# Optimization experiments

Measured on AMD Instinct MI355X. Metric: run time of the kernel, lower is better.

## Reference

```python
import jax, jax.numpy as jnp
import numpy as np

B, L, H, E = 2, 2048, 16, 64  # S == L (causal self-attention), D == E


def setup_inputs() -> dict:
    key = jax.random.key(0)
    kq, kk, kv, ks = jax.random.split(key, 4)
    queries = jax.random.normal(kq, (B, L, H, E), dtype=jnp.float32)
    keys = jax.random.normal(kk, (B, L, H, E), dtype=jnp.float32)
    values = jax.random.normal(kv, (B, L, H, E), dtype=jnp.float32)
    # TriangularCausalMask: True above the diagonal -> masked out
    attn_mask = jnp.broadcast_to(
        jnp.triu(jnp.ones((L, L), dtype=bool), k=1)[None, None], (B, 1, L, L)
    )
    init_score = jax.random.uniform(ks, (B, L, L), dtype=jnp.float32)
    return {
        "queries": queries,
        "keys": keys,
        "values": values,
        "attn_mask": attn_mask,
        "init_score": init_score,
    }


def reference(queries, keys, values, attn_mask, init_score):
    # queries: [B,L,H,E], keys: [B,S,H,E], values: [B,S,H,D]
    E_ = queries.shape[-1]
    scale = 1.0 / np.sqrt(E_).astype(np.float32)
    # scores: [B,H,L,S]
    scores = jnp.einsum('blhe,bshe->bhls', queries, keys)
    scores = jnp.where(attn_mask, -jnp.inf, scores)
    A = jax.nn.softmax(scale * scores, axis=-1)  # dropout p=0 -> identity
    # post-softmax bias, broadcast over heads
    A = A + 0.1 * init_score[:, None, :, :]
    # V: [B,L,H,D]
    V = jnp.einsum('bhls,bshd->blhd', A, values)
    return V
```

## Files before the change

### kernel.cpp

```cpp
#include <hip/hip_runtime.h>
#include <hip/hip_bf16.h>
#include <math.h>

#define BB 2
#define LL 2048
#define HH 16
#define EE 64
#define LOG2E 1.44269504089f

typedef __attribute__((ext_vector_type(8))) short short8;
typedef __attribute__((ext_vector_type(4))) float floatx4;
typedef unsigned int u32;

union S8 { short8 v; u32 u[4]; ushort4 q[2]; };

__device__ inline u32 pkbf(float lo, float hi) {
    union { __hip_bfloat162 h; u32 u; } c;
    c.h = __float22bfloat162_rn(make_float2(lo, hi));
    return c.u;
}

__device__ inline ushort4 cvt4(float4 v) {
    union { __hip_bfloat162 h; u32 u; } a, b;
    a.h = __float22bfloat162_rn(make_float2(v.x, v.y));
    b.h = __float22bfloat162_rn(make_float2(v.z, v.w));
    ushort4 r;
    r.x = (unsigned short)(a.u & 0xffffu);
    r.y = (unsigned short)(a.u >> 16);
    r.z = (unsigned short)(b.u & 0xffffu);
    r.w = (unsigned short)(b.u >> 16);
    return r;
}

__device__ inline short8 pack8(float4 a, float4 b) {
    S8 s; s.q[0] = cvt4(a); s.q[1] = cvt4(b); return s.v;
}

__device__ inline void async16(unsigned short* lds, const unsigned short* g) {
    __builtin_amdgcn_global_load_lds(
        (const __attribute__((address_space(1))) u32*)g,
        (__attribute__((address_space(3))) u32*)lds, 16, 0, 0);
}

__global__ __launch_bounds__(256) void prepass(
    const float* __restrict__ k, const float* __restrict__ v,
    const float* __restrict__ isc, unsigned short* __restrict__ kb,
    unsigned short* __restrict__ vt, unsigned short* __restrict__ isb)
{
    const int bid = blockIdx.x;
    const int t = threadIdx.x;
    if (bid < 1024) {
        #pragma unroll
        for (int it = 0; it < 2; ++it) {
            int idx = bid * 512 + it * 256 + t;
            const float4* src = (const float4*)k + idx * 2;
            float4 a = src[0], c = src[1];
            int e8 = idx & 7, h = (idx >> 3) & 15, l = (idx >> 7) & 2047, b = idx >> 18;
            *(short8*)&kb[(((b * 16 + h) * 2048 + l) * 64) + e8 * 8] = pack8(a, c);
        }
    } else if (bid < 2048) {
        __shared__ float Tf[64][69];
        const int vb = bid - 1024;
        const int st = vb & 31, h = (vb >> 5) & 15, b = vb >> 9;
        const int s0 = st * 64;
        #pragma unroll
        for (int i = 0; i < 4; ++i) {
            int r = i * 16 + (t >> 4), c = (t & 15) * 4;
            float4 val = *(const float4*)(v + (((b * LL + s0 + r) * HH + h) * EE) + c);
            *(float4*)&Tf[r][c] = val;
        }
        __syncthreads();
        #pragma unroll
        for (int i = 0; i < 2; ++i) {
            int slot = t + i * 256;
            int d = slot >> 3, s8 = (slot & 7) * 8;
            float4 lo = make_float4(Tf[s8 + 0][d], Tf[s8 + 1][d],
                                    Tf[s8 + 2][d], Tf[s8 + 3][d]);
            float4 hi = make_float4(Tf[s8 + 4][d], Tf[s8 + 5][d],
                                    Tf[s8 + 6][d], Tf[s8 + 7][d]);
            *(short8*)&vt[((b * 16 + h) * 64 + d) * 2048 + s0 + s8] = pack8(lo, hi);
        }
    } else {
        const int ib = bid - 2048;
        #pragma unroll
        for (int it = 0; it < 4; ++it) {
            int idx = ib * 1024 + it * 256 + t;
            const float4* src = (const float4*)isc + idx * 2;
            float4 a = src[0], c = src[1];
            a.x *= 0.1f; a.y *= 0.1f; a.z *= 0.1f; a.w *= 0.1f;
            c.x *= 0.1f; c.y *= 0.1f; c.z *= 0.1f; c.w *= 0.1f;
            ((short8*)isb)[idx] = pack8(a, c);
        }
    }
}

template <int MODE>
__device__ __forceinline__ void tile_step(
    const unsigned short* __restrict__ Ks, const unsigned short* __restrict__ Vs,
    const short8 qf[2], const short8 isf[2], const short8 ones,
    floatx4 o_attn[4], floatx4 o_bias[4], floatx4& o_sum,
    int s0, int mbase, int wave, int lq, int ln, int lnl,
    int alo, int ahi, bool hisel)
{
    u32 pk[4][2];
    if (MODE < 2) {
        #pragma unroll
        for (int sb = 0; sb < 4; ++sb) {
            if (MODE == 1 && wave < sb) { pk[sb][0] = 0; pk[sb][1] = 0; continue; }
            short8 kf0 = *(const short8*)&Ks[(sb * 16 + ln) * 64 + ((lq ^ lnl) << 3)];
            short8 kf1 = *(const short8*)&Ks[(sb * 16 + ln) * 64 + (((4 + lq) ^ lnl) << 3)];
            floatx4 sa = {0.f, 0.f, 0.f, 0.f};
            __builtin_amdgcn_s_setprio(1);
            sa = __builtin_amdgcn_mfma_f32_16x16x32_bf16(kf0, qf[0], sa, 0, 0, 0);
            sa = __builtin_amdgcn_mfma_f32_16x16x32_bf16(kf1, qf[1], sa, 0, 0, 0);
            __builtin_amdgcn_s_setprio(0);
            float pv[4];
            #pragma unroll
            for (int r = 0; r < 4; ++r) {
                float t = sa[r];
                if (MODE == 1 && (s0 + sb * 16 + lq * 4 + r) > (mbase + ln)) t = -INFINITY;
                pv[r] = exp2f(t);
            }
            pk[sb][0] = pkbf(pv[0], pv[1]);
            pk[sb][1] = pkbf(pv[2], pv[3]);
        }
    }
    #pragma unroll
    for (int kk = 0; kk < 2; ++kk) {
        short8 vf[4];
        #pragma unroll
        for (int db = 0; db < 4; ++db)
            vf[db] = *(const short8*)&Vs[(db * 16 + ln) * 64 + (((kk * 4 + lq) ^ lnl) << 3)];
        short8 af = isf[kk];
        __builtin_amdgcn_s_setprio(1);
        #pragma unroll
        for (int db = 0; db < 4; ++db)
            o_bias[db] = __builtin_amdgcn_mfma_f32_16x16x32_bf16(af, vf[db], o_bias[db], 0, 0, 0);
        __builtin_amdgcn_s_setprio(0);
        if (MODE < 2) {
            S8 pf;
            u32 a0 = (u32)__builtin_amdgcn_ds_bpermute(alo, (int)pk[kk * 2][0]);
            u32 b0 = (u32)__builtin_amdgcn_ds_bpermute(alo, (int)pk[kk * 2 + 1][0]);
            pf.u[0] = hisel ? b0 : a0;
            u32 a1 = (u32)__builtin_amdgcn_ds_bpermute(alo, (int)pk[kk * 2][1]);
            u32 b1 = (u32)__builtin_amdgcn_ds_bpermute(alo, (int)pk[kk * 2 + 1][1]);
            pf.u[1] = hisel ? b1 : a1;
            u32 a2 = (u32)__builtin_amdgcn_ds_bpermute(ahi, (int)pk[kk * 2][0]);
            u32 b2 = (u32)__builtin_amdgcn_ds_bpermute(ahi, (int)pk[kk * 2 + 1][0]);
            pf.u[2] = hisel ? b2 : a2;
            u32 a3 = (u32)__builtin_amdgcn_ds_bpermute(ahi, (int)pk[kk * 2][1]);
            u32 b3 = (u32)__builtin_amdgcn_ds_bpermute(ahi, (int)pk[kk * 2 + 1][1]);
            pf.u[3] = hisel ? b3 : a3;
            __builtin_amdgcn_s_setprio(1);
            o_sum = __builtin_amdgcn_mfma_f32_16x16x32_bf16(pf.v, ones, o_sum, 0, 0, 0);
            #pragma unroll
            for (int db = 0; db < 4; ++db)
                o_attn[db] = __builtin_amdgcn_mfma_f32_16x16x32_bf16(pf.v, vf[db], o_attn[db], 0, 0, 0);
            __builtin_amdgcn_s_setprio(0);
        }
    }
}

__global__ __launch_bounds__(256, 4) void fused10(
    const float* __restrict__ q, const unsigned short* __restrict__ kb,
    const unsigned short* __restrict__ vt, const unsigned short* __restrict__ isb,
    float* __restrict__ out)
{
    __shared__ unsigned short Ks[2][64 * 64];
    __shared__ unsigned short Vs[2][64 * 64];

    const int tid = threadIdx.x, lane = tid & 63, wave = tid >> 6;
    const int lq = lane >> 4, ln = lane & 15, lnl = ln & 7;

    const int bid = blockIdx.x;
    const int h = bid & 15, b = (bid >> 4) & 1, g = bid >> 5;
    int qt;
    if (g < 8) qt = 31 - g;
    else if (g < 16) qt = g;
    else if (g < 24) qt = 39 - g;
    else qt = g - 24;
    const int q0 = qt * 64;
    const int mbase = q0 + wave * 16;

    short8 qf[2];
    {
        const float sc = 0.125f * LOG2E;
        const float* qrow = q + (((long)(b * LL + mbase + ln)) * HH + h) * EE;
        #pragma unroll
        for (int kk = 0; kk < 2; ++kk) {
            float4 a = *(const float4*)(qrow + kk * 32 + lq * 8);
            float4 c = *(const float4*)(qrow + kk * 32 + lq * 8 + 4);
            a.x *= sc; a.y *= sc; a.z *= sc; a.w *= sc;
            c.x *= sc; c.y *= sc; c.z *= sc; c.w *= sc;
            qf[kk] = pack8(a, c);
        }
    }

    const unsigned short* kbh = kb + (long)(b * HH + h) * (LL * EE);
    const unsigned short* vth = vt + (long)(b * HH + h) * (EE * LL);

    floatx4 o_attn[4], o_bias[4];
    #pragma unroll
    for (int db = 0; db < 4; ++db) {
        o_attn[db] = (floatx4){0.f, 0.f, 0.f, 0.f};
        o_bias[db] = (floatx4){0.f, 0.f, 0.f, 0.f};
    }
    floatx4 o_sum = (floatx4){0.f, 0.f, 0.f, 0.f};
    const short8 ones = {(short)0x3F80, (short)0x3F80, (short)0x3F80, (short)0x3F80,
                         (short)0x3F80, (short)0x3F80, (short)0x3F80, (short)0x3F80};

    const int rr = lane >> 3, jl = lane & 7;
    const int swz = (jl ^ rr) * 8;
    const unsigned short* ksrc0 = kbh + (wave * 16 + rr) * 64 + swz;
    const unsigned short* ksrc1 = kbh + (wave * 16 + 8 + rr) * 64 + swz;
    const unsigned short* vsrc0 = vth + (wave * 16 + rr) * LL + swz;
    const unsigned short* vsrc1 = vth + (wave * 16 + 8 + rr) * LL + swz;

    const unsigned short* isrow =
        isb + (long)(b * LL + q0 + wave * 16 + ln) * LL + lq * 8;

    const int alo = (((lq & 1) * 2) * 16 + ln) * 4;
    const int ahi = (((lq & 1) * 2 + 1) * 16 + ln) * 4;
    const bool hisel = (lq >= 2);

    auto issue = [&](int j) {
        const int s0 = j * 64, bsel = j & 1;
        if (j <= qt) {
            async16(&Ks[bsel][(wave * 16) * 64], ksrc0 + s0 * 64);
            async16(&Ks[bsel][(wave * 16 + 8) * 64], ksrc1 + s0 * 64);
        }
        async16(&Vs[bsel][(wave * 16) * 64], vsrc0 + s0);
        async16(&Vs[bsel][(wave * 16 + 8) * 64], vsrc1 + s0);
    };

    short8 isf[2], isfn[2];
    auto ldnext = [&](int j, short8* dst) {
        int jc = j < 32 ? j : 31;
        dst[0] = *(const short8*)(isrow + jc * 64);
        dst[1] = *(const short8*)(isrow + jc * 64 + 32);
    };

    ldnext(0, isf);
    issue(0);
    for (int j = 0; j < qt; ++j) {
        __syncthreads();
        issue(j + 1);
        ldnext(j + 1, isfn);
        tile_step<0>(Ks[j & 1], Vs[j & 1], qf, isf, ones, o_attn, o_bias, o_sum,
                     j * 64, mbase, wave, lq, ln, lnl, alo, ahi, hisel);
        isf[0] = isfn[0]; isf[1] = isfn[1];
    }
    {
        __syncthreads();
        if (qt < 31) issue(qt + 1);
        ldnext(qt + 1, isfn);
        tile_step<1>(Ks[qt & 1], Vs[qt & 1], qf, isf, ones, o_attn, o_bias, o_sum,
                     q0, mbase, wave, lq, ln, lnl, alo, ahi, hisel);
        isf[0] = isfn[0]; isf[1] = isfn[1];
    }
    for (int j = qt + 1; j < 32; ++j) {
        __syncthreads();
        if (j < 31) issue(j + 1);
        ldnext(j + 1, isfn);
        tile_step<2>(Vs[j & 1], Vs[j & 1], qf, isf, ones, o_attn, o_bias, o_sum,
                     j * 64, mbase, wave, lq, ln, lnl, alo, ahi, hisel);
        isf[0] = isfn[0]; isf[1] = isfn[1];
    }

    #pragma unroll
    for (int r = 0; r < 4; ++r) {
        float inv = 1.0f / o_sum[r];
        int m = mbase + lq * 4 + r;
        float* ob = out + (((long)(b * LL + m)) * HH + h) * EE;
        #pragma unroll
        for (int db = 0; db < 4; ++db)
            ob[db * 16 + ln] = o_attn[db][r] * inv + o_bias[db][r];
    }
}

extern "C" void kernel_launch(void* const* d_in, const int* in_sizes, int n_in,
                              void* d_out, int out_size, void* d_ws, size_t ws_size,
                              hipStream_t stream) {
    (void)in_sizes; (void)n_in; (void)out_size; (void)ws_size;
    const float* q   = (const float*)d_in[0];
    const float* k   = (const float*)d_in[1];
    const float* v   = (const float*)d_in[2];
    const float* isc = (const float*)d_in[4];
    float* out = (float*)d_out;

    unsigned short* kb  = (unsigned short*)d_ws;
    unsigned short* vt  = (unsigned short*)((char*)d_ws + (8u << 20));
    unsigned short* isb = (unsigned short*)((char*)d_ws + (16u << 20));

    prepass<<<dim3(3072), dim3(256), 0, stream>>>(k, v, isc, kb, vt, isb);
    fused10<<<dim3(1024), dim3(256), 0, stream>>>(q, kb, vt, isb, out);
}
```

Before: 196.4 us.

## Pair complementary causal query tiles per block to share K/V tile loads

Each block now processes two query tiles (qt=31-p and qt=p) together, so every K/V tile loaded into shared memory serves both, halving K/V staging traffic and balancing causal work per block. The grid halves to 512 blocks and launch bounds drop to 2 blocks per CU, since per-thread accumulators roughly double. The cost is higher register pressure and lower occupancy, with fewer blocks available to hide latency.

```diff
diff --git a/kernel.cpp b/kernel.cpp
--- a/kernel.cpp
+++ b/kernel.cpp
@@ -94,35 +94,63 @@
     }
 }
 
-template <int MODE>
-__device__ __forceinline__ void tile_step(
+template <int MA, int MB>
+__device__ __forceinline__ void tile_pair(
     const unsigned short* __restrict__ Ks, const unsigned short* __restrict__ Vs,
-    const short8 qf[2], const short8 isf[2], const short8 ones,
-    floatx4 o_attn[4], floatx4 o_bias[4], floatx4& o_sum,
-    int s0, int mbase, int wave, int lq, int ln, int lnl,
+    const short8 qfA[2], const short8 qfB[2],
+    const short8 isfA[2], const short8 isfB[2], const short8 ones,
+    floatx4 oaA[4], floatx4 obA[4], floatx4& osA,
+    floatx4 oaB[4], floatx4 obB[4], floatx4& osB,
+    int s0, int mbaseA, int mbaseB, int wave, int lq, int ln, int lnl,
     int alo, int ahi, bool hisel)
 {
-    u32 pk[4][2];
-    if (MODE < 2) {
+    u32 pkA[4][2], pkB[4][2];
+    if (MA < 2) {
         #pragma unroll
         for (int sb = 0; sb < 4; ++sb) {
-            if (MODE == 1 && wave < sb) { pk[sb][0] = 0; pk[sb][1] = 0; continue; }
+            const bool needA = (MA == 0) || (wave >= sb);
+            const bool needB = (MB == 0) || (MB == 1 && wave >= sb);
+            if (!needA && !needB) {
+                pkA[sb][0] = 0; pkA[sb][1] = 0;
+                if (MB < 2) { pkB[sb][0] = 0; pkB[sb][1] = 0; }
+                continue;
+            }
             short8 kf0 = *(const short8*)&Ks[(sb * 16 + ln) * 64 + ((lq ^ lnl) << 3)];
             short8 kf1 = *(const short8*)&Ks[(sb * 16 + ln) * 64 + (((4 + lq) ^ lnl) << 3)];
-            floatx4 sa = {0.f, 0.f, 0.f, 0.f};
-            __builtin_amdgcn_s_setprio(1);
-            sa = __builtin_amdgcn_mfma_f32_16x16x32_bf16(kf0, qf[0], sa, 0, 0, 0);
-            sa = __builtin_amdgcn_mfma_f32_16x16x32_bf16(kf1, qf[1], sa, 0, 0, 0);
-            __builtin_amdgcn_s_setprio(0);
-            float pv[4];
-            #pragma unroll
-            for (int r = 0; r < 4; ++r) {
-                float t = sa[r];
-                if (MODE == 1 && (s0 + sb * 16 + lq * 4 + r) > (mbase + ln)) t = -INFINITY;
-                pv[r] = exp2f(t);
+            if (needA) {
+                floatx4 sa = {0.f, 0.f, 0.f, 0.f};
+                __builtin_amdgcn_s_setprio(1);
+                sa = __builtin_amdgcn_mfma_f32_16x16x32_bf16(kf0, qfA[0], sa, 0, 0, 0);
+                sa = __builtin_amdgcn_mfma_f32_16x16x32_bf16(kf1, qfA[1], sa, 0, 0, 0);
+                __builtin_amdgcn_s_setprio(0);
+                float pv[4];
+                #pragma unroll
+                for (int r = 0; r < 4; ++r) {
+                    float t = sa[r];
+                    if (MA == 1 && (s0 + sb * 16 + lq * 4 + r) > (mbaseA + ln)) t = -INFINITY;
+                    pv[r] = exp2f(t);
+                }
+                pkA[sb][0] = pkbf(pv[0], pv[1]);
+                pkA[sb][1] = pkbf(pv[2], pv[3]);
+            } else { pkA[sb][0] = 0; pkA[sb][1] = 0; }
+            if (MB < 2) {
+                if (needB) {
+                    floatx4 sa = {0.f, 0.f, 0.f, 0.f};
+                    __builtin_amdgcn_s_setprio(1);
+                    sa = __builtin_amdgcn_mfma_f32_16x16x32_bf16(kf0, qfB[0], sa, 0, 0, 0);
+                    sa = __builtin_amdgcn_mfma_f32_16x16x32_bf16(kf1, qfB[1], sa, 0, 0, 0);
+                    __builtin_amdgcn_s_setprio(0);
+                    float pv[4];
+                    #pragma unroll
+                    for (int r = 0; r < 4; ++r) {
+                        float t = sa[r];
+                        if (MB == 1 && (s0 + sb * 16 + lq * 4 + r) > (mbaseB + ln)) t = -INFINITY;
+                        pv[r] = exp2f(t);
+                    }
+                    pkB[sb][0] = pkbf(pv[0], pv[1]);
+                    pkB[sb][1] = pkbf(pv[2], pv[3]);
+                } else { pkB[sb][0] = 0; pkB[sb][1] = 0; }
             }
-            pk[sb][0] = pkbf(pv[0], pv[1]);
-            pk[sb][1] = pkbf(pv[2], pv[3]);
         }
     }
     #pragma unroll
@@ -131,37 +159,60 @@
         #pragma unroll
         for (int db = 0; db < 4; ++db)
             vf[db] = *(const short8*)&Vs[(db * 16 + ln) * 64 + (((kk * 4 + lq) ^ lnl) << 3)];
-        short8 af = isf[kk];
         __builtin_amdgcn_s_setprio(1);
         #pragma unroll
         for (int db = 0; db < 4; ++db)
-            o_bias[db] = __builtin_amdgcn_mfma_f32_16x16x32_bf16(af, vf[db], o_bias[db], 0, 0, 0);
+            obA[db] = __builtin_amdgcn_mfma_f32_16x16x32_bf16(isfA[kk], vf[db], obA[db], 0, 0, 0);
+        #pragma unroll
+        for (int db = 0; db < 4; ++db)
+            obB[db] = __builtin_amdgcn_mfma_f32_16x16x32_bf16(isfB[kk], vf[db], obB[db], 0, 0, 0);
         __builtin_amdgcn_s_setprio(0);
-        if (MODE < 2) {
+        if (MA < 2) {
             S8 pf;
-            u32 a0 = (u32)__builtin_amdgcn_ds_bpermute(alo, (int)pk[kk * 2][0]);
-            u32 b0 = (u32)__builtin_amdgcn_ds_bpermute(alo, (int)pk[kk * 2 + 1][0]);
+            u32 a0 = (u32)__builtin_amdgcn_ds_bpermute(alo, (int)pkA[kk * 2][0]);
+            u32 b0 = (u32)__builtin_amdgcn_ds_bpermute(alo, (int)pkA[kk * 2 + 1][0]);
             pf.u[0] = hisel ? b0 : a0;
-            u32 a1 = (u32)__builtin_amdgcn_ds_bpermute(alo, (int)pk[kk * 2][1]);
-            u32 b1 = (u32)__builtin_amdgcn_ds_bpermute(alo, (int)pk[kk * 2 + 1][1]);
+            u32 a1 = (u32)__builtin_amdgcn_ds_bpermute(alo, (int)pkA[kk * 2][1]);
+            u32 b1 = (u32)__builtin_amdgcn_ds_bpermute(alo, (int)pkA[kk * 2 + 1][1]);
             pf.u[1] = hisel ? b1 : a1;
-            u32 a2 = (u32)__builtin_amdgcn_ds_bpermute(ahi, (int)pk[kk * 2][0]);
-            u32 b2 = (u32)__builtin_amdgcn_ds_bpermute(ahi, (int)pk[kk * 2 + 1][0]);
+            u32 a2 = (u32)__builtin_amdgcn_ds_bpermute(ahi, (int)pkA[kk * 2][0]);
+            u32 b2 = (u32)__builtin_amdgcn_ds_bpermute(ahi, (int)pkA[kk * 2 + 1][0]);
             pf.u[2] = hisel ? b2 : a2;
-            u32 a3 = (u32)__builtin_amdgcn_ds_bpermute(ahi, (int)pk[kk * 2][1]);
-            u32 b3 = (u32)__builtin_amdgcn_ds_bpermute(ahi, (int)pk[kk * 2 + 1][1]);
+            u32 a3 = (u32)__builtin_amdgcn_ds_bpermute(ahi, (int)pkA[kk * 2][1]);
+            u32 b3 = (u32)__builtin_amdgcn_ds_bpermute(ahi, (int)pkA[kk * 2 + 1][1]);
             pf.u[3] = hisel ? b3 : a3;
             __builtin_amdgcn_s_setprio(1);
-            o_sum = __builtin_amdgcn_mfma_f32_16x16x32_bf16(pf.v, ones, o_sum, 0, 0, 0);
+            osA = __builtin_amdgcn_mfma_f32_16x16x32_bf16(pf.v, ones, osA, 0, 0, 0);
             #pragma unroll
             for (int db = 0; db < 4; ++db)
-                o_attn[db] = __builtin_amdgcn_mfma_f32_16x16x32_bf16(pf.v, vf[db], o_attn[db], 0, 0, 0);
+                oaA[db] = __builtin_amdgcn_mfma_f32_16x16x32_bf16(pf.v, vf[db], oaA[db], 0, 0, 0);
             __builtin_amdgcn_s_setprio(0);
         }
-    }
-}
-
-__global__ __launch_bounds__(256, 4) void fused10(
+        if (MB < 2) {
+            S8 pf;
+            u32 a0 = (u32)__builtin_amdgcn_ds_bpermute(alo, (int)pkB[kk * 2][0]);
+            u32 b0 = (u32)__builtin_amdgcn_ds_bpermute(alo, (int)pkB[kk * 2 + 1][0]);
+            pf.u[0] = hisel ? b0 : a0;
+            u32 a1 = (u32)__builtin_amdgcn_ds_bpermute(alo, (int)pkB[kk * 2][1]);
+            u32 b1 = (u32)__builtin_amdgcn_ds_bpermute(alo, (int)pkB[kk * 2 + 1][1]);
+            pf.u[1] = hisel ? b1 : a1;
+            u32 a2 = (u32)__builtin_amdgcn_ds_bpermute(ahi, (int)pkB[kk * 2][0]);
+            u32 b2 = (u32)__builtin_amdgcn_ds_bpermute(ahi, (int)pkB[kk * 2 + 1][0]);
+            pf.u[2] = hisel ? b2 : a2;
+            u32 a3 = (u32)__builtin_amdgcn_ds_bpermute(ahi, (int)pkB[kk * 2][1]);
+            u32 b3 = (u32)__builtin_amdgcn_ds_bpermute(ahi, (int)pkB[kk * 2 + 1][1]);
+            pf.u[3] = hisel ? b3 : a3;
+            __builtin_amdgcn_s_setprio(1);
+            osB = __builtin_amdgcn_mfma_f32_16x16x32_bf16(pf.v, ones, osB, 0, 0, 0);
+            #pragma unroll
+            for (int db = 0; db < 4; ++db)
+                oaB[db] = __builtin_amdgcn_mfma_f32_16x16x32_bf16(pf.v, vf[db], oaB[db], 0, 0, 0);
+            __builtin_amdgcn_s_setprio(0);
+        }
+    }
+}
+
+__global__ __launch_bounds__(256, 2) void fused12(
     const float* __restrict__ q, const unsigned short* __restrict__ kb,
     const unsigned short* __restrict__ vt, const unsigned short* __restrict__ isb,
     float* __restrict__ out)
@@ -173,39 +224,44 @@
     const int lq = lane >> 4, ln = lane & 15, lnl = ln & 7;
 
     const int bid = blockIdx.x;
-    const int h = bid & 15, b = (bid >> 4) & 1, g = bid >> 5;
-    int qt;
-    if (g < 8) qt = 31 - g;
-    else if (g < 16) qt = g;
-    else if (g < 24) qt = 39 - g;
-    else qt = g - 24;
-    const int q0 = qt * 64;
-    const int mbase = q0 + wave * 16;
-
-    short8 qf[2];
+    const int h = bid & 15, b = (bid >> 4) & 1, p = bid >> 5;
+    const int qtA = 31 - p, qtB = p;
+    const int q0A = qtA * 64, q0B = qtB * 64;
+    const int mbaseA = q0A + wave * 16, mbaseB = q0B + wave * 16;
+
+    short8 qfA[2], qfB[2];
     {
         const float sc = 0.125f * LOG2E;
-        const float* qrow = q + (((long)(b * LL + mbase + ln)) * HH + h) * EE;
+        const float* qrowA = q + (((long)(b * LL + mbaseA + ln)) * HH + h) * EE;
+        const float* qrowB = q + (((long)(b * LL + mbaseB + ln)) * HH + h) * EE;
         #pragma unroll
         for (int kk = 0; kk < 2; ++kk) {
-            float4 a = *(const float4*)(qrow + kk * 32 + lq * 8);
-            float4 c = *(const float4*)(qrow + kk * 32 + lq * 8 + 4);
+            float4 a = *(const float4*)(qrowA + kk * 32 + lq * 8);
+            float4 c = *(const float4*)(qrowA + kk * 32 + lq * 8 + 4);
             a.x *= sc; a.y *= sc; a.z *= sc; a.w *= sc;
             c.x *= sc; c.y *= sc; c.z *= sc; c.w *= sc;
-            qf[kk] = pack8(a, c);
+            qfA[kk] = pack8(a, c);
+            float4 d = *(const float4*)(qrowB + kk * 32 + lq * 8);
+            float4 e = *(const float4*)(qrowB + kk * 32 + lq * 8 + 4);
+            d.x *= sc; d.y *= sc; d.z *= sc; d.w *= sc;
+            e.x *= sc; e.y *= sc; e.z *= sc; e.w *= sc;
+            qfB[kk] = pack8(d, e);
         }
     }
 
     const unsigned short* kbh = kb + (long)(b * HH + h) * (LL * EE);
     const unsigned short* vth = vt + (long)(b * HH + h) * (EE * LL);
 
-    floatx4 o_attn[4], o_bias[4];
+    floatx4 oaA[4], obA[4], oaB[4], obB[4];
     #pragma unroll
     for (int db = 0; db < 4; ++db) {
-        o_attn[db] = (floatx4){0.f, 0.f, 0.f, 0.f};
-        o_bias[db] = (floatx4){0.f, 0.f, 0.f, 0.f};
-    }
-    floatx4 o_sum = (floatx4){0.f, 0.f, 0.f, 0.f};
+        oaA[db] = (floatx4){0.f, 0.f, 0.f, 0.f};
+        obA[db] = (floatx4){0.f, 0.f, 0.f, 0.f};
+        oaB[db] = (floatx4){0.f, 0.f, 0.f, 0.f};
+        obB[db] = (floatx4){0.f, 0.f, 0.f, 0.f};
+    }
+    floatx4 osA = (floatx4){0.f, 0.f, 0.f, 0.f};
+    floatx4 osB = (floatx4){0.f, 0.f, 0.f, 0.f};
     const short8 ones = {(short)0x3F80, (short)0x3F80, (short)0x3F80, (short)0x3F80,
                          (short)0x3F80, (short)0x3F80, (short)0x3F80, (short)0x3F80};
 
@@ -216,8 +272,10 @@
     const unsigned short* vsrc0 = vth + (wave * 16 + rr) * LL + swz;
     const unsigned short* vsrc1 = vth + (wave * 16 + 8 + rr) * LL + swz;
 
-    const unsigned short* isrow =
-        isb + (long)(b * LL + q0 + wave * 16 + ln) * LL + lq * 8;
+    const unsigned short* isrowA =
+        isb + (long)(b * LL + q0A + wave * 16 + ln) * LL + lq * 8;
+    const unsigned short* isrowB =
+        isb + (long)(b * LL + q0B + wave * 16 + ln) * LL + lq * 8;
 
     const int alo = (((lq & 1) * 2) * 16 + ln) * 4;
     const int ahi = (((lq & 1) * 2 + 1) * 16 + ln) * 4;
@@ -225,7 +283,7 @@
 
     auto issue = [&](int j) {
         const int s0 = j * 64, bsel = j & 1;
-        if (j <= qt) {
+        if (j <= qtA) {
             async16(&Ks[bsel][(wave * 16) * 64], ksrc0 + s0 * 64);
             async16(&Ks[bsel][(wave * 16 + 8) * 64], ksrc1 + s0 * 64);
         }
@@ -233,48 +291,59 @@
         async16(&Vs[bsel][(wave * 16 + 8) * 64], vsrc1 + s0);
     };
 
-    short8 isf[2], isfn[2];
-    auto ldnext = [&](int j, short8* dst) {
+    short8 isfA[2], isfB[2], isfnA[2], isfnB[2];
+    auto ldnext = [&](int j, const unsigned short* isrow, short8* dst) {
         int jc = j < 32 ? j : 31;
         dst[0] = *(const short8*)(isrow + jc * 64);
         dst[1] = *(const short8*)(isrow + jc * 64 + 32);
     };
 
-    ldnext(0, isf);
+    ldnext(0, isrowA, isfA);
+    ldnext(0, isrowB, isfB);
     issue(0);
-    for (int j = 0; j < qt; ++j) {
-        __syncthreads();
-        issue(j + 1);
-        ldnext(j + 1, isfn);
-        tile_step<0>(Ks[j & 1], Vs[j & 1], qf, isf, ones, o_attn, o_bias, o_sum,
-                     j * 64, mbase, wave, lq, ln, lnl, alo, ahi, hisel);
-        isf[0] = isfn[0]; isf[1] = isfn[1];
-    }
-    {
-        __syncthreads();
-        if (qt < 31) issue(qt + 1);
-        ldnext(qt + 1, isfn);
-        tile_step<1>(Ks[qt & 1], Vs[qt & 1], qf, isf, ones, o_attn, o_bias, o_sum,
-                     q0, mbase, wave, lq, ln, lnl, alo, ahi, hisel);
-        isf[0] = isfn[0]; isf[1] = isfn[1];
-    }
-    for (int j = qt + 1; j < 32; ++j) {
+    for (int j = 0; j < 32; ++j) {
         __syncthreads();
         if (j < 31) issue(j + 1);
-        ldnext(j + 1, isfn);
-        tile_step<2>(Vs[j & 1], Vs[j & 1], qf, isf, ones, o_attn, o_bias, o_sum,
-                     j * 64, mbase, wave, lq, ln, lnl, alo, ahi, hisel);
-        isf[0] = isfn[0]; isf[1] = isfn[1];
+        ldnext(j + 1, isrowA, isfnA);
+        ldnext(j + 1, isrowB, isfnB);
+        const int m3 = j & 1;
+        if (j < qtB)
+            tile_pair<0, 0>(Ks[m3], Vs[m3], qfA, qfB, isfA, isfB, ones,
+                            oaA, obA, osA, oaB, obB, osB,
+                            j * 64, mbaseA, mbaseB, wave, lq, ln, lnl, alo, ahi, hisel);
+        else if (j == qtB)
+            tile_pair<0, 1>(Ks[m3], Vs[m3], qfA, qfB, isfA, isfB, ones,
+                            oaA, obA, osA, oaB, obB, osB,
+                            j * 64, mbaseA, mbaseB, wave, lq, ln, lnl, alo, ahi, hisel);
+        else if (j < qtA)
+            tile_pair<0, 2>(Ks[m3], Vs[m3], qfA, qfB, isfA, isfB, ones,
+                            oaA, obA, osA, oaB, obB, osB,
+                            j * 64, mbaseA, mbaseB, wave, lq, ln, lnl, alo, ahi, hisel);
+        else if (j == qtA)
+            tile_pair<1, 2>(Ks[m3], Vs[m3], qfA, qfB, isfA, isfB, ones,
+                            oaA, obA, osA, oaB, obB, osB,
+                            j * 64, mbaseA, mbaseB, wave, lq, ln, lnl, alo, ahi, hisel);
+        else
+            tile_pair<2, 2>(Ks[m3], Vs[m3], qfA, qfB, isfA, isfB, ones,
+                            oaA, obA, osA, oaB, obB, osB,
+                            j * 64, mbaseA, mbaseB, wave, lq, ln, lnl, alo, ahi, hisel);
+        isfA[0] = isfnA[0]; isfA[1] = isfnA[1];
+        isfB[0] = isfnB[0]; isfB[1] = isfnB[1];
     }
 
     #pragma unroll
     for (int r = 0; r < 4; ++r) {
-        float inv = 1.0f / o_sum[r];
-        int m = mbase + lq * 4 + r;
-        float* ob = out + (((long)(b * LL + m)) * HH + h) * EE;
-        #pragma unroll
-        for (int db = 0; db < 4; ++db)
-            ob[db * 16 + ln] = o_attn[db][r] * inv + o_bias[db][r];
+        float invA = 1.0f / osA[r];
+        float invB = 1.0f / osB[r];
+        int mA = mbaseA + lq * 4 + r;
+        int mB = mbaseB + lq * 4 + r;
+        float* obpA = out + (((long)(b * LL + mA)) * HH + h) * EE;
+        float* obpB = out + (((long)(b * LL + mB)) * HH + h) * EE;
+        #pragma unroll
+        for (int db = 0; db < 4; ++db) {
+            obpA[db * 16 + ln] = oaA[db][r] * invA + obA[db][r];
+            obpB[db * 16 + ln] = oaB[db][r] * invB + obB[db][r];
+        }
     }
 }
 
@@ -293,5 +362,5 @@
     unsigned short* isb = (unsigned short*)((char*)d_ws + (16u << 20));
 
     prepass<<<dim3(3072), dim3(256), 0, stream>>>(k, v, isc, kb, vt, isb);
-    fused10<<<dim3(1024), dim3(256), 0, stream>>>(q, kb, vt, isb, out);
-}
+    fused12<<<dim3(512), dim3(256), 0, stream>>>(q, kb, vt, isb, out);
+}
```

Result: slower. 218.3 us (+11.2%).
